# Kernel optimization log

Hardware: AMD Instinct MI355X
Metric: run time of the kernel (lower is better)

Reference implementation:

```python
import jax, jax.numpy as jnp
import numpy as np

B, N = 32, 512            # batch, max nodes per graph
F_DIM, M_DIM = 1024, 256  # node feature dim, first hidden dim
N_SEM = 8                 # number of semantic-class experts
XYZ, DIM_E = 3, 8
OUT_SIZE = 2 * XYZ + DIM_E  # 14 (default reg branch)
EPS = 1e-8                # padding value used by out_seq_to_batch


def setup_inputs() -> dict:
    key = jax.random.key(0)
    ks = jax.random.split(key, 12)
    def w(k, shape, fan_in):
        return jax.random.normal(k, shape, jnp.float32) / np.float32(np.sqrt(fan_in))
    return {
        "nodes": jax.random.normal(ks[0], (B, N, F_DIM), jnp.float32),
        "sem": jax.random.randint(ks[1], (B, N), 0, N_SEM, jnp.int32),
        "lengths": jax.random.randint(ks[2], (B,), 64, N + 1, jnp.int32),
        # y expert MLPs (4 layers), stacked over experts
        "W1": w(ks[3], (N_SEM, F_DIM, M_DIM), F_DIM), "b1": jnp.zeros((N_SEM, M_DIM), jnp.float32),
        "W2": w(ks[4], (N_SEM, M_DIM, 64), M_DIM),   "b2": jnp.zeros((N_SEM, 64), jnp.float32),
        "W3": w(ks[5], (N_SEM, 64, 32), 64),         "b3": jnp.zeros((N_SEM, 32), jnp.float32),
        "W4": w(ks[6], (N_SEM, 32, OUT_SIZE), 32),   "b4": jnp.zeros((N_SEM, OUT_SIZE), jnp.float32),
        # rot expert MLPs (2 layers), stacked over experts
        "R1": w(ks[7], (N_SEM, F_DIM, M_DIM), F_DIM), "rb1": jnp.zeros((N_SEM, M_DIM), jnp.float32),
        "R2": w(ks[8], (N_SEM, M_DIM, XYZ), M_DIM),   "rb2": jnp.zeros((N_SEM, XYZ), jnp.float32),
    }


def _prim_mlps(nodes, sem, lengths, W1, b1, W2, b2, W3, b3, W4, b4, R1, rb1, R2, rb2):
    Bn, Nn, Fd = nodes.shape
    x = nodes.reshape(-1, Fd)                       # [T, F], T = B*N tokens
    semf = sem.reshape(-1)                          # [T] expert id per token
    # dense dispatch: run every expert on all tokens, then select per token
    h1 = jax.nn.relu(jnp.einsum('tf,efm->etm', x, W1) + b1[:, None, :])   # [E,T,M]
    h2 = jax.nn.relu(jnp.einsum('etm,emh->eth', h1, W2) + b2[:, None, :]) # [E,T,64]
    h3 = jax.nn.relu(jnp.einsum('eth,ehg->etg', h2, W3) + b3[:, None, :]) # [E,T,32]
    y_all = jnp.einsum('etg,ego->eto', h3, W4) + b4[:, None, :]           # [E,T,OUT]
    r1 = jax.nn.relu(jnp.einsum('tf,efm->etm', x, R1) + rb1[:, None, :])  # [E,T,M]
    rot_all = jnp.einsum('etm,emo->eto', r1, R2) + rb2[:, None, :]        # [E,T,XYZ]
    t = jnp.arange(x.shape[0])
    y = y_all[semf, t]                              # [T, OUT]
    rot = rot_all[semf, t]                          # [T, XYZ]
    out = jnp.concatenate([y, rot], axis=-1).reshape(Bn, Nn, -1)
    # positions beyond each graph's length are filled with eps (out_seq_to_batch)
    mask = (jnp.arange(Nn)[None, :] < lengths[:, None])[:, :, None]
    return jnp.where(mask, out, jnp.float32(EPS))


def reference(nodes, sem, lengths, W1, b1, W2, b2, W3, b3, W4, b4, R1, rb1, R2, rb2):
    return _prim_mlps(nodes, sem, lengths, W1, b1, W2, b2, W3, b3, W4, b4,
                      R1, rb1, R2, rb2)
```

## Files before the change

kernel.cpp:

```cpp
#include <hip/hip_runtime.h>
#include <stdint.h>

#define T_TOK 16384
#define NE 8
#define EPSV 1e-8f
#define MAXC128 136
#define MAXC64  264
#define MAXC16  1032

#define WS_PERM   0
#define WS_PART   65536
#define WS_OFFS   67584
#define WS_XS     131072
#define WS_WT     (WS_XS + 16512*1024*2)
#define WS_H1     (WS_WT + 8*512*1024*2)
#define WS_W2T    (WS_H1 + 16448*512*2)
#define WS_W3T    (WS_W2T + 8*64*256*2)
#define WS_W4T    (WS_W3T + 8*32*64*2)
#define WS_R2T    (WS_W4T + 8*16*32*2)

typedef __attribute__((ext_vector_type(8))) short bf16x8;
typedef __attribute__((ext_vector_type(4))) float f32x4;

__device__ __forceinline__ unsigned short f2bf(float f) {
    unsigned u = __float_as_uint(f);
    u += 0x7fffu + ((u >> 16) & 1u);
    return (unsigned short)(u >> 16);
}

__device__ __forceinline__ void gl_lds16(const void* g, void* l) {
    __builtin_amdgcn_global_load_lds(
        (const __attribute__((address_space(1))) void*)g,
        (__attribute__((address_space(3))) void*)l,
        16, 0, 0);
}

__device__ __forceinline__ bool chunk_lookup(const int* __restrict__ offs, int c, int csize,
                                             int& e, int& base, int& len) {
    int acc = 0;
#pragma unroll
    for (int i = 0; i < NE; i++) {
        int s = offs[i], t = offs[i + 1];
        int cc = (t - s + csize - 1) / csize;
        if (c < acc + cc) {
            e = i;
            base = s + (c - acc) * csize;
            len = (t - base < csize) ? (t - base) : csize;
            return true;
        }
        acc += cc;
    }
    return false;
}

__global__ __launch_bounds__(256) void k_prep1(const float* __restrict__ W1,
                                               const float* __restrict__ R1,
                                               const float* __restrict__ W2,
                                               const float* __restrict__ W3,
                                               const float* __restrict__ W4,
                                               const float* __restrict__ R2,
                                               const int* __restrict__ sem,
                                               unsigned short* __restrict__ wt,
                                               unsigned short* __restrict__ w2t,
                                               unsigned short* __restrict__ w3t,
                                               unsigned short* __restrict__ w4t,
                                               unsigned short* __restrict__ r2t,
                                               int* __restrict__ ws_i) {
    __shared__ float tile[64][65];
    int id = blockIdx.x, tid = threadIdx.x;
    if (id >= 1024) {
        __shared__ int cnt[NE];
        int hb = id - 1024, lane = tid & 63;
        if (tid < NE) cnt[tid] = 0;
        __syncthreads();
        int s = sem[hb * 256 + tid];
#pragma unroll
        for (int e = 0; e < NE; e++) {
            unsigned long long m = __ballot(s == e);
            if (lane == e) atomicAdd(&cnt[e], (int)__popcll(m));
        }
        __syncthreads();
        if (tid < NE) ws_i[(WS_PART >> 2) + hb * NE + tid] = cnt[tid];
        return;
    }
    int e = id >> 7, rem = id & 127;
    int ny = rem >> 4, kx = rem & 15;
    int k0 = kx * 64, n0 = ny * 64;
    const float* src = (n0 < 256) ? (W1 + (size_t)e * 1024 * 256 + n0)
                                  : (R1 + (size_t)e * 1024 * 256 + (n0 - 256));
    int rr = tid >> 4;
    int cg = (tid & 15) * 4;
#pragma unroll
    for (int p = 0; p < 4; p++) {
        int kk = p * 16 + rr;
        float4 v = *(const float4*)(src + (size_t)(k0 + kk) * 256 + cg);
        tile[kk][cg] = v.x; tile[kk][cg + 1] = v.y; tile[kk][cg + 2] = v.z; tile[kk][cg + 3] = v.w;
    }
    __syncthreads();
    int nn = tid >> 3;
    int k8 = tid & 7;
#pragma unroll
    for (int p = 0; p < 2; p++) {
        int n = p * 32 + nn;
        unsigned w[4];
#pragma unroll
        for (int j = 0; j < 4; j++) {
            float f0 = tile[k8 * 8 + 2 * j][n];
            float f1 = tile[k8 * 8 + 2 * j + 1][n];
            w[j] = (unsigned)f2bf(f0) | ((unsigned)f2bf(f1) << 16);
        }
        *(uint4*)(wt + (size_t)(e * 512 + n0 + n) * 1024 + k0 + k8 * 8) =
            make_uint4(w[0], w[1], w[2], w[3]);
    }
    if (ny == 0) {
        int x = kx;
        for (int j = tid; j < 1024; j += 256) {
            int idx = x * 1024 + j; int k = idx & 255, n = idx >> 8;
            w2t[(size_t)(e * 64 + n) * 256 + k] = f2bf(W2[(size_t)e * 16384 + k * 64 + n]);
        }
        if (tid < 128) {
            int idx = x * 128 + tid; int k = idx & 63, n = idx >> 6;
            w3t[(size_t)(e * 32 + n) * 64 + k] = f2bf(W3[(size_t)e * 2048 + k * 32 + n]);
        }
        if (tid < 32) {
            int idx = x * 32 + tid; int k = idx & 31, n = idx >> 5;
            w4t[(size_t)(e * 16 + n) * 32 + k] = (n < 14) ? f2bf(W4[(size_t)e * 448 + k * 14 + n])
                                                          : (unsigned short)0;
        }
        {
            int idx = x * 256 + tid; int k = idx & 255, n = idx >> 8;
            r2t[(size_t)(e * 16 + n) * 256 + k] = (n < 3) ? f2bf(R2[(size_t)e * 768 + k * 3 + n])
                                                          : (unsigned short)0;
        }
    }
}

__global__ __launch_bounds__(256) void k_scatter(const int* __restrict__ sem,
                                                 const float* __restrict__ nodes,
                                                 int* __restrict__ ws_i,
                                                 unsigned short* __restrict__ xs) {
    __shared__ int parts[512];
    __shared__ int tot[NE], preb[NE], ebase[NE + 1];
    __shared__ int wcnt[4][NE];
    __shared__ int destS[256];
    int b = blockIdx.x, g = b >> 3, j = b & 7;
    int tid = threadIdx.x, wave = tid >> 6, lane = tid & 63;
    parts[tid] = ws_i[(WS_PART >> 2) + tid];
    parts[256 + tid] = ws_i[(WS_PART >> 2) + 256 + tid];
    __syncthreads();
    if (tid < NE) {
        int t = 0, p = 0;
        for (int bb = 0; bb < 64; bb++) {
            int v = parts[bb * NE + tid];
            t += v;
            if (bb < g) p += v;
        }
        tot[tid] = t; preb[tid] = p;
    }
    __syncthreads();
    if (tid == 0) {
        int base = 0;
        for (int e = 0; e < NE; e++) { ebase[e] = base; base += tot[e]; }
        ebase[NE] = base;
        if (b == 0)
            for (int e = 0; e <= NE; e++) ws_i[(WS_OFFS >> 2) + e] = ebase[e];
    }
    int i = g * 256 + tid;
    int s = sem[i];
    int rank = 0;
#pragma unroll
    for (int e = 0; e < NE; e++) {
        unsigned long long m = __ballot(s == e);
        if (s == e) rank = (int)__popcll(m & ((1ull << lane) - 1ull));
        if (lane == e) wcnt[wave][e] = (int)__popcll(m);
    }
    __syncthreads();
    int wpre = 0;
#pragma unroll
    for (int w = 0; w < 4; w++)
        if (w < wave) wpre += wcnt[w][s];
    int dest = ebase[s] + preb[s] + wpre + rank;
    destS[tid] = dest;
    if (j == 0) ws_i[(WS_PERM >> 2) + dest] = i;
    __syncthreads();
#pragma unroll 4
    for (int r = j * 32; r < j * 32 + 32; r++) {
        int tok = g * 256 + r;
        int d = destS[r];
        float4 v = *(const float4*)(nodes + (size_t)tok * 1024 + tid * 4);
        unsigned p0 = (unsigned)f2bf(v.x) | ((unsigned)f2bf(v.y) << 16);
        unsigned p1 = (unsigned)f2bf(v.z) | ((unsigned)f2bf(v.w) << 16);
        *(uint2*)(xs + (size_t)d * 1024 + tid * 4) = make_uint2(p0, p1);
    }
}

__global__ __launch_bounds__(256) void k_gemm(const unsigned short* __restrict__ xs,
                                              const unsigned short* __restrict__ wt,
                                              const float* __restrict__ b1,
                                              const float* __restrict__ rb1,
                                              const int* __restrict__ ws_i,
                                              unsigned short* __restrict__ h1) {
    __shared__ __align__(16) short As[2][64 * 64];
    __shared__ __align__(16) short Bs[2][128 * 64];
    int e, base, len;
    if (!chunk_lookup(ws_i + (WS_OFFS >> 2), blockIdx.x, 64, e, base, len)) return;
    int n0 = blockIdx.y * 128;
    int tid = threadIdx.x;
    int wave = tid >> 6, lane = tid & 63;
    int quad = lane >> 4, lr = lane & 15;
    int wn = wave * 32;

    f32x4 acc[4][2];
#pragma unroll
    for (int i = 0; i < 4; i++)
#pragma unroll
        for (int j = 0; j < 2; j++) acc[i][j] = (f32x4){0.f, 0.f, 0.f, 0.f};

    const unsigned short* Ag = xs + (size_t)base * 1024;
    const unsigned short* Bg = wt + (size_t)(e * 512 + n0) * 1024;

    const unsigned short* srcA[2];
    int dstA[2];
#pragma unroll
    for (int i = 0; i < 2; i++) {
        int s = i * 256 + wave * 64 + lane;
        int r = s >> 3, cs = (s & 7) ^ (r & 7);
        srcA[i] = Ag + (size_t)r * 1024 + cs * 8;
        dstA[i] = (i * 256 + wave * 64) * 8;
    }
    const unsigned short* srcB[4];
    int dstB[4];
#pragma unroll
    for (int i = 0; i < 4; i++) {
        int s = i * 256 + wave * 64 + lane;
        int r = s >> 3, cs = (s & 7) ^ (r & 7);
        srcB[i] = Bg + (size_t)r * 1024 + cs * 8;
        dstB[i] = (i * 256 + wave * 64) * 8;
    }

#pragma unroll
    for (int i = 0; i < 2; i++) gl_lds16(srcA[i], &As[0][dstA[i]]);
#pragma unroll
    for (int i = 0; i < 4; i++) gl_lds16(srcB[i], &Bs[0][dstB[i]]);

    for (int kb = 0; kb < 16; kb++) {
        int cur = kb & 1;
        if (kb < 15) {
            int nxt = cur ^ 1;
#pragma unroll
            for (int i = 0; i < 2; i++) gl_lds16(srcA[i] + (kb + 1) * 64, &As[nxt][dstA[i]]);
#pragma unroll
            for (int i = 0; i < 4; i++) gl_lds16(srcB[i] + (kb + 1) * 64, &Bs[nxt][dstB[i]]);
            asm volatile("s_waitcnt vmcnt(6)" ::: "memory");
        } else {
            asm volatile("s_waitcnt vmcnt(0)" ::: "memory");
        }
        __builtin_amdgcn_sched_barrier(0);
        __builtin_amdgcn_s_barrier();

        const short* Ab = As[cur];
        const short* Bb = Bs[cur];
        bf16x8 af[2][4], bfr[2][2];
#pragma unroll
        for (int im = 0; im < 4; im++) {
            int r = im * 16 + lr;
#pragma unroll
            for (int kh = 0; kh < 2; kh++) {
                int q = kh * 4 + quad;
                af[kh][im] = *(const bf16x8*)(Ab + (r * 8 + (q ^ (r & 7))) * 8);
            }
        }
#pragma unroll
        for (int in = 0; in < 2; in++) {
            int r = wn + in * 16 + lr;
#pragma unroll
            for (int kh = 0; kh < 2; kh++) {
                int q = kh * 4 + quad;
                bfr[kh][in] = *(const bf16x8*)(Bb + (r * 8 + (q ^ (r & 7))) * 8);
            }
        }
#pragma unroll
        for (int kh = 0; kh < 2; kh++)
#pragma unroll
            for (int im = 0; im < 4; im++)
#pragma unroll
                for (int in = 0; in < 2; in++)
                    acc[im][in] = __builtin_amdgcn_mfma_f32_16x16x32_bf16(af[kh][im], bfr[kh][in], acc[im][in], 0, 0, 0);

        if (kb < 15) {
            __builtin_amdgcn_sched_barrier(0);
            __builtin_amdgcn_s_barrier();
        }
    }

#pragma unroll
    for (int in = 0; in < 2; in++) {
        int gcol = n0 + wn + in * 16 + lr;
        float bias = (gcol < 256) ? b1[e * 256 + gcol] : rb1[e * 256 + gcol - 256];
#pragma unroll
        for (int im = 0; im < 4; im++) {
#pragma unroll
            for (int v = 0; v < 4; v++) {
                int r = im * 16 + quad * 4 + v;
                if (r < len) {
                    float val = fmaxf(acc[im][in][v] + bias, 0.f);
                    h1[(size_t)(base + r) * 512 + gcol] = f2bf(val);
                }
            }
        }
    }
}

__global__ __launch_bounds__(256) void k_tail(const unsigned short* __restrict__ h1,
                                              const int* __restrict__ ws_i,
                                              const unsigned short* __restrict__ w2t,
                                              const unsigned short* __restrict__ w3t,
                                              const unsigned short* __restrict__ w4t,
                                              const unsigned short* __restrict__ r2t,
                                              const float* __restrict__ b2,
                                              const float* __restrict__ b3,
                                              const float* __restrict__ b4,
                                              const float* __restrict__ rb2,
                                              const int* __restrict__ lengths,
                                              float* __restrict__ out) {
    __shared__ __align__(16) unsigned short h2s[16][64];
    __shared__ __align__(16) unsigned short h3s[16][32];

    int e, base, len;
    if (!chunk_lookup(ws_i + (WS_OFFS >> 2), blockIdx.x, 16, e, base, len)) return;
    int tid = threadIdx.x, wave = tid >> 6, lane = tid & 63;
    int quad = lane >> 4, lr = lane & 15;
    int lead = blockIdx.x & 3;

    const unsigned short* Ap = h1 + (size_t)base * 512;

    f32x4 acc2;
    { float bb = b2[e * 64 + wave * 16 + lr]; acc2 = (f32x4){bb, bb, bb, bb}; }
    f32x4 accr;
    { float bb = (lr < 3) ? rb2[e * 3 + lr] : 0.f; accr = (f32x4){bb, bb, bb, bb}; }

    const unsigned short* W2e = w2t + (size_t)e * 64 * 256;
    const unsigned short* R2e = r2t + (size_t)e * 16 * 256;
#pragma unroll
    for (int kk = 0; kk < 8; kk++) {
        int k0 = kk * 32;
        bf16x8 a = *(const bf16x8*)(Ap + lr * 512 + k0 + quad * 8);
        bf16x8 b = *(const bf16x8*)(W2e + (wave * 16 + lr) * 256 + k0 + quad * 8);
        acc2 = __builtin_amdgcn_mfma_f32_16x16x32_bf16(a, b, acc2, 0, 0, 0);
        if (wave == lead) {
            bf16x8 ar = *(const bf16x8*)(Ap + lr * 512 + 256 + k0 + quad * 8);
            bf16x8 br = *(const bf16x8*)(R2e + lr * 256 + k0 + quad * 8);
            accr = __builtin_amdgcn_mfma_f32_16x16x32_bf16(ar, br, accr, 0, 0, 0);
        }
    }
#pragma unroll
    for (int v = 0; v < 4; v++)
        h2s[quad * 4 + v][wave * 16 + lr] = f2bf(fmaxf(acc2[v], 0.f));
    __syncthreads();
    if (wave != lead) return;

    f32x4 acc3[2];
#pragma unroll
    for (int t = 0; t < 2; t++) {
        float bb = b3[e * 32 + t * 16 + lr];
        acc3[t] = (f32x4){bb, bb, bb, bb};
    }
    const unsigned short* W3e = w3t + (size_t)e * 32 * 64;
#pragma unroll
    for (int kk = 0; kk < 2; kk++) {
        int k0 = kk * 32;
        bf16x8 a = *(const bf16x8*)(&h2s[lr][k0 + quad * 8]);
#pragma unroll
        for (int t = 0; t < 2; t++) {
            bf16x8 b = *(const bf16x8*)(W3e + (t * 16 + lr) * 64 + k0 + quad * 8);
            acc3[t] = __builtin_amdgcn_mfma_f32_16x16x32_bf16(a, b, acc3[t], 0, 0, 0);
        }
    }
#pragma unroll
    for (int t = 0; t < 2; t++)
#pragma unroll
        for (int v = 0; v < 4; v++)
            h3s[quad * 4 + v][t * 16 + lr] = f2bf(fmaxf(acc3[t][v], 0.f));

    f32x4 acc4;
    { float bb = (lr < 14) ? b4[e * 14 + lr] : 0.f; acc4 = (f32x4){bb, bb, bb, bb}; }
    {
        bf16x8 a = *(const bf16x8*)(&h3s[lr][quad * 8]);
        bf16x8 b = *(const bf16x8*)(w4t + ((size_t)e * 16 + lr) * 32 + quad * 8);
        acc4 = __builtin_amdgcn_mfma_f32_16x16x32_bf16(a, b, acc4, 0, 0, 0);
    }

    const int* perm = ws_i + (WS_PERM >> 2);
#pragma unroll
    for (int v = 0; v < 4; v++) {
        int t = quad * 4 + v;
        if (t < len) {
            int token = perm[base + t];
            int bi = token >> 9, ni = token & 511;
            int valid = ni < lengths[bi];
            if (lr < 14) out[(size_t)token * 17 + lr] = valid ? acc4[v] : EPSV;
            if (lr < 3)  out[(size_t)token * 17 + 14 + lr] = valid ? accr[v] : EPSV;
        }
    }
}

extern "C" void kernel_launch(void* const* d_in, const int* in_sizes, int n_in,
                              void* d_out, int out_size, void* d_ws, size_t ws_size,
                              hipStream_t stream) {
    (void)in_sizes; (void)n_in; (void)out_size; (void)ws_size;
    const float* nodes   = (const float*)d_in[0];
    const int*   sem     = (const int*)d_in[1];
    const int*   lengths = (const int*)d_in[2];
    const float* W1 = (const float*)d_in[3];
    const float* b1 = (const float*)d_in[4];
    const float* W2 = (const float*)d_in[5];
    const float* b2 = (const float*)d_in[6];
    const float* W3 = (const float*)d_in[7];
    const float* b3 = (const float*)d_in[8];
    const float* W4 = (const float*)d_in[9];
    const float* b4 = (const float*)d_in[10];
    const float* R1  = (const float*)d_in[11];
    const float* rb1 = (const float*)d_in[12];
    const float* R2  = (const float*)d_in[13];
    const float* rb2 = (const float*)d_in[14];
    float* out = (float*)d_out;

    char* ws = (char*)d_ws;
    int* ws_i = (int*)ws;
    unsigned short* xs  = (unsigned short*)(ws + WS_XS);
    unsigned short* wt  = (unsigned short*)(ws + WS_WT);
    unsigned short* h1  = (unsigned short*)(ws + WS_H1);
    unsigned short* w2t = (unsigned short*)(ws + WS_W2T);
    unsigned short* w3t = (unsigned short*)(ws + WS_W3T);
    unsigned short* w4t = (unsigned short*)(ws + WS_W4T);
    unsigned short* r2t = (unsigned short*)(ws + WS_R2T);

    hipLaunchKernelGGL(k_prep1, dim3(1088), dim3(256), 0, stream,
                       W1, R1, W2, W3, W4, R2, sem, wt, w2t, w3t, w4t, r2t, ws_i);
    hipLaunchKernelGGL(k_scatter, dim3(512), dim3(256), 0, stream, sem, nodes, ws_i, xs);
    hipLaunchKernelGGL(k_gemm, dim3(MAXC64, 4), dim3(256), 0, stream,
                       (const unsigned short*)xs, (const unsigned short*)wt, b1, rb1,
                       (const int*)ws_i, h1);
    hipLaunchKernelGGL(k_tail, dim3(MAXC16), dim3(256), 0, stream,
                       (const unsigned short*)h1, (const int*)ws_i,
                       (const unsigned short*)w2t, (const unsigned short*)w3t,
                       (const unsigned short*)w4t, (const unsigned short*)r2t,
                       b2, b3, b4, rb2, lengths, out);
}
```

Measured before the change: 192.2 us.

## Fuse fp32-to-bf16 gather of tokens into the first-layer GEMM A-tile load

Measured after the change: 205.5 us. 6.9% more time.

```diff
diff --git a/kernel.cpp b/kernel.cpp
--- a/kernel.cpp
+++ b/kernel.cpp
@@ -4,15 +4,13 @@
 #define T_TOK 16384
 #define NE 8
 #define EPSV 1e-8f
-#define MAXC128 136
 #define MAXC64  264
 #define MAXC16  1032
 
 #define WS_PERM   0
 #define WS_PART   65536
 #define WS_OFFS   67584
-#define WS_XS     131072
-#define WS_WT     (WS_XS + 16512*1024*2)
+#define WS_WT     131072
 #define WS_H1     (WS_WT + 8*512*1024*2)
 #define WS_W2T    (WS_H1 + 16448*512*2)
 #define WS_W3T    (WS_W2T + 8*64*256*2)
@@ -26,6 +24,14 @@
     unsigned u = __float_as_uint(f);
     u += 0x7fffu + ((u >> 16) & 1u);
     return (unsigned short)(u >> 16);
+}
+
+__device__ __forceinline__ void cvt_wr16(short* dst, float4 a, float4 b) {
+    unsigned u0 = (unsigned)f2bf(a.x) | ((unsigned)f2bf(a.y) << 16);
+    unsigned u1 = (unsigned)f2bf(a.z) | ((unsigned)f2bf(a.w) << 16);
+    unsigned u2 = (unsigned)f2bf(b.x) | ((unsigned)f2bf(b.y) << 16);
+    unsigned u3 = (unsigned)f2bf(b.z) | ((unsigned)f2bf(b.w) << 16);
+    *(uint4*)dst = make_uint4(u0, u1, u2, u3);
 }
 
 __device__ __forceinline__ void gl_lds16(const void* g, void* l) {
@@ -135,15 +141,12 @@
     }
 }
 
-__global__ __launch_bounds__(256) void k_scatter(const int* __restrict__ sem,
-                                                 const float* __restrict__ nodes,
-                                                 int* __restrict__ ws_i,
-                                                 unsigned short* __restrict__ xs) {
+__global__ __launch_bounds__(256) void k_perm(const int* __restrict__ sem,
+                                              int* __restrict__ ws_i) {
     __shared__ int parts[512];
     __shared__ int tot[NE], preb[NE], ebase[NE + 1];
     __shared__ int wcnt[4][NE];
-    __shared__ int destS[256];
-    int b = blockIdx.x, g = b >> 3, j = b & 7;
+    int g = blockIdx.x;
     int tid = threadIdx.x, wave = tid >> 6, lane = tid & 63;
     parts[tid] = ws_i[(WS_PART >> 2) + tid];
     parts[256 + tid] = ws_i[(WS_PART >> 2) + 256 + tid];
@@ -162,7 +165,7 @@
         int base = 0;
         for (int e = 0; e < NE; e++) { ebase[e] = base; base += tot[e]; }
         ebase[NE] = base;
-        if (b == 0)
+        if (g == 0)
             for (int e = 0; e <= NE; e++) ws_i[(WS_OFFS >> 2) + e] = ebase[e];
     }
     int i = g * 256 + tid;
@@ -180,21 +183,10 @@
     for (int w = 0; w < 4; w++)
         if (w < wave) wpre += wcnt[w][s];
     int dest = ebase[s] + preb[s] + wpre + rank;
-    destS[tid] = dest;
-    if (j == 0) ws_i[(WS_PERM >> 2) + dest] = i;
-    __syncthreads();
-#pragma unroll 4
-    for (int r = j * 32; r < j * 32 + 32; r++) {
-        int tok = g * 256 + r;
-        int d = destS[r];
-        float4 v = *(const float4*)(nodes + (size_t)tok * 1024 + tid * 4);
-        unsigned p0 = (unsigned)f2bf(v.x) | ((unsigned)f2bf(v.y) << 16);
-        unsigned p1 = (unsigned)f2bf(v.z) | ((unsigned)f2bf(v.w) << 16);
-        *(uint2*)(xs + (size_t)d * 1024 + tid * 4) = make_uint2(p0, p1);
-    }
-}
-
-__global__ __launch_bounds__(256) void k_gemm(const unsigned short* __restrict__ xs,
+    ws_i[(WS_PERM >> 2) + dest] = i;
+}
+
+__global__ __launch_bounds__(256) void k_gemm(const float* __restrict__ nodes,
                                               const unsigned short* __restrict__ wt,
                                               const float* __restrict__ b1,
                                               const float* __restrict__ rb1,
@@ -202,9 +194,12 @@
                                               unsigned short* __restrict__ h1) {
     __shared__ __align__(16) short As[2][64 * 64];
     __shared__ __align__(16) short Bs[2][128 * 64];
+    int bid = blockIdx.x;
+    int wgid = (bid & 7) * ((MAXC64 * 4) / 8) + (bid >> 3);
+    int c = wgid >> 2, nblk = wgid & 3;
     int e, base, len;
-    if (!chunk_lookup(ws_i + (WS_OFFS >> 2), blockIdx.x, 64, e, base, len)) return;
-    int n0 = blockIdx.y * 128;
+    if (!chunk_lookup(ws_i + (WS_OFFS >> 2), c, 64, e, base, len)) return;
+    int n0 = nblk * 128;
     int tid = threadIdx.x;
     int wave = tid >> 6, lane = tid & 63;
     int quad = lane >> 4, lr = lane & 15;
@@ -216,17 +211,20 @@
 #pragma unroll
         for (int j = 0; j < 2; j++) acc[i][j] = (f32x4){0.f, 0.f, 0.f, 0.f};
 
-    const unsigned short* Ag = xs + (size_t)base * 1024;
+    const int* perm = ws_i + (WS_PERM >> 2);
     const unsigned short* Bg = wt + (size_t)(e * 512 + n0) * 1024;
 
-    const unsigned short* srcA[2];
+    const float* apA[2];
     int dstA[2];
 #pragma unroll
     for (int i = 0; i < 2; i++) {
-        int s = i * 256 + wave * 64 + lane;
+        int s = i * 256 + tid;
         int r = s >> 3, cs = (s & 7) ^ (r & 7);
-        srcA[i] = Ag + (size_t)r * 1024 + cs * 8;
-        dstA[i] = (i * 256 + wave * 64) * 8;
+        int gidx = base + r;
+        if (gidx > T_TOK - 1) gidx = T_TOK - 1;
+        int tok = perm[gidx];
+        apA[i] = nodes + (size_t)tok * 1024 + cs * 8;
+        dstA[i] = s * 8;
     }
     const unsigned short* srcB[4];
     int dstB[4];
@@ -238,25 +236,30 @@
         dstB[i] = (i * 256 + wave * 64) * 8;
     }
 
-#pragma unroll
-    for (int i = 0; i < 2; i++) gl_lds16(srcA[i], &As[0][dstA[i]]);
+    float4 fa0, fb0, fa1, fb1;
+
+    fa0 = *(const float4*)(apA[0]); fb0 = *(const float4*)(apA[0] + 4);
+    fa1 = *(const float4*)(apA[1]); fb1 = *(const float4*)(apA[1] + 4);
 #pragma unroll
     for (int i = 0; i < 4; i++) gl_lds16(srcB[i], &Bs[0][dstB[i]]);
+    cvt_wr16(&As[0][dstA[0]], fa0, fb0);
+    cvt_wr16(&As[0][dstA[1]], fa1, fb1);
+    asm volatile("s_waitcnt vmcnt(0) lgkmcnt(0)" ::: "memory");
+    __builtin_amdgcn_sched_barrier(0);
+    __builtin_amdgcn_s_barrier();
 
     for (int kb = 0; kb < 16; kb++) {
         int cur = kb & 1;
+        int nxt = cur ^ 1;
         if (kb < 15) {
-            int nxt = cur ^ 1;
-#pragma unroll
-            for (int i = 0; i < 2; i++) gl_lds16(srcA[i] + (kb + 1) * 64, &As[nxt][dstA[i]]);
+            fa0 = *(const float4*)(apA[0] + (kb + 1) * 64);
+            fb0 = *(const float4*)(apA[0] + (kb + 1) * 64 + 4);
+            fa1 = *(const float4*)(apA[1] + (kb + 1) * 64);
+            fb1 = *(const float4*)(apA[1] + (kb + 1) * 64 + 4);
 #pragma unroll
             for (int i = 0; i < 4; i++) gl_lds16(srcB[i] + (kb + 1) * 64, &Bs[nxt][dstB[i]]);
-            asm volatile("s_waitcnt vmcnt(6)" ::: "memory");
-        } else {
-            asm volatile("s_waitcnt vmcnt(0)" ::: "memory");
         }
         __builtin_amdgcn_sched_barrier(0);
-        __builtin_amdgcn_s_barrier();
 
         const short* Ab = As[cur];
         const short* Bb = Bs[cur];
@@ -288,6 +291,9 @@
                     acc[im][in] = __builtin_amdgcn_mfma_f32_16x16x32_bf16(af[kh][im], bfr[kh][in], acc[im][in], 0, 0, 0);
 
         if (kb < 15) {
+            cvt_wr16(&As[nxt][dstA[0]], fa0, fb0);
+            cvt_wr16(&As[nxt][dstA[1]], fa1, fb1);
+            asm volatile("s_waitcnt vmcnt(0) lgkmcnt(0)" ::: "memory");
             __builtin_amdgcn_sched_barrier(0);
             __builtin_amdgcn_s_barrier();
         }
@@ -427,7 +433,6 @@
 
     char* ws = (char*)d_ws;
     int* ws_i = (int*)ws;
-    unsigned short* xs  = (unsigned short*)(ws + WS_XS);
     unsigned short* wt  = (unsigned short*)(ws + WS_WT);
     unsigned short* h1  = (unsigned short*)(ws + WS_H1);
     unsigned short* w2t = (unsigned short*)(ws + WS_W2T);
@@ -437,10 +442,9 @@
 
     hipLaunchKernelGGL(k_prep1, dim3(1088), dim3(256), 0, stream,
                        W1, R1, W2, W3, W4, R2, sem, wt, w2t, w3t, w4t, r2t, ws_i);
-    hipLaunchKernelGGL(k_scatter, dim3(512), dim3(256), 0, stream, sem, nodes, ws_i, xs);
-    hipLaunchKernelGGL(k_gemm, dim3(MAXC64, 4), dim3(256), 0, stream,
-                       (const unsigned short*)xs, (const unsigned short*)wt, b1, rb1,
-                       (const int*)ws_i, h1);
+    hipLaunchKernelGGL(k_perm, dim3(64), dim3(256), 0, stream, sem, ws_i);
+    hipLaunchKernelGGL(k_gemm, dim3(MAXC64 * 4), dim3(256), 0, stream,
+                       nodes, (const unsigned short*)wt, b1, rb1, (const int*)ws_i, h1);
     hipLaunchKernelGGL(k_tail, dim3(MAXC16), dim3(256), 0, stream,
                        (const unsigned short*)h1, (const int*)ws_i,
                        (const unsigned short*)w2t, (const unsigned short*)w3t,
```
